# Kernel optimization log

Measured on AMD Instinct MI355X. Metric: run time of the kernel, lower is better.

## Reference

```python
import jax, jax.numpy as jnp
import numpy as np
import math

D_MODEL = 1024
N_HEADS = 16
D_HEAD = 64
GROUP_SIZE = 2
N_GROUPS = N_HEADS // GROUP_SIZE
D_MLP = 4096
BATCH = 2
SEQ = 2048
LN_EPS = 1e-5


def setup_inputs() -> dict:
    key = jax.random.key(0)
    ks = jax.random.split(key, 12)

    def xavier(k, shape):
        # torch xavier_uniform on a 3D tensor treats dim0 as fan_in, prod(rest) as fan_out
        fan_in = shape[0]
        fan_out = int(np.prod(shape[1:]))
        bound = math.sqrt(6.0 / (fan_in + fan_out))
        return jax.random.uniform(k, shape, jnp.float32, -bound, bound)

    def linear_w(k, out_f, in_f):
        bound = 1.0 / math.sqrt(in_f)
        return jax.random.uniform(k, (out_f, in_f), jnp.float32, -bound, bound)

    return {
        "x": jax.random.normal(ks[0], (BATCH, SEQ, D_MODEL), jnp.float32),
        "ln1_w": jnp.ones((D_MODEL,), jnp.float32),
        "ln1_b": jnp.zeros((D_MODEL,), jnp.float32),
        "W_Q": xavier(ks[1], (D_MODEL, N_HEADS, D_HEAD)),
        "W_K": xavier(ks[2], (D_MODEL, N_GROUPS, D_HEAD)),
        "W_V": xavier(ks[3], (D_MODEL, N_GROUPS, D_HEAD)),
        "W_out": xavier(ks[4], (D_HEAD, N_HEADS, D_MODEL)),
        "b_out": jnp.zeros((D_MODEL,), jnp.float32),
        "ln2_w": jnp.ones((D_MODEL,), jnp.float32),
        "ln2_b": jnp.zeros((D_MODEL,), jnp.float32),
        "mlp1_w": linear_w(ks[5], D_MLP, D_MODEL),
        "mlp1_b": jax.random.uniform(ks[6], (D_MLP,), jnp.float32, -1.0 / math.sqrt(D_MODEL), 1.0 / math.sqrt(D_MODEL)),
        "mlp2_w": linear_w(ks[7], D_MODEL, D_MLP),
        "mlp2_b": jax.random.uniform(ks[8], (D_MODEL,), jnp.float32, -1.0 / math.sqrt(D_MLP), 1.0 / math.sqrt(D_MLP)),
    }


def _layernorm(x, w, b):
    mu = jnp.mean(x, axis=-1, keepdims=True)
    var = jnp.var(x, axis=-1, keepdims=True)
    return (x - mu) * jax.lax.rsqrt(var + LN_EPS) * w + b


def _gqa_attention(resid, W_Q, W_K, W_V, W_out, b_out):
    b, s, _ = resid.shape
    q = jnp.einsum("bsd,dhk->bshk", resid, W_Q)            # [b, s, n_heads, d_head]
    q = q.reshape(b, s, N_GROUPS, GROUP_SIZE, D_HEAD)      # [b, s, g, gs, k]
    k = jnp.einsum("bsd,dgk->bsgk", resid, W_K)            # [b, s, g, k]
    v = jnp.einsum("bsd,dgk->bsgk", resid, W_V)
    scores = jnp.einsum("bqgik,btgk->bgiqt", q, k) / math.sqrt(D_HEAD)  # [b, g, gs, q, t]
    causal_mask = jnp.triu(jnp.ones((s, s), dtype=bool), k=1)
    scores = jnp.where(causal_mask, jnp.float32(-1000000.0), scores)
    probs = jax.nn.softmax(scores, axis=-1)
    z = jnp.einsum("bgiqt,btgk->bqgik", probs, v)          # [b, q, g, gs, k]
    z = z.reshape(b, s, N_HEADS, D_HEAD)
    return jnp.einsum("bshk,khd->bsd", z, W_out) + b_out


def reference(x, ln1_w, ln1_b, W_Q, W_K, W_V, W_out, b_out,
              ln2_w, ln2_b, mlp1_w, mlp1_b, mlp2_w, mlp2_b):
    normed = _layernorm(x, ln1_w, ln1_b)
    attn_out = _gqa_attention(normed, W_Q, W_K, W_V, W_out, b_out)
    post_attn = x + attn_out
    h = _layernorm(post_attn, ln2_w, ln2_b)
    h = jax.nn.gelu(h @ mlp1_w.T + mlp1_b, approximate=False)  # torch nn.GELU default = exact erf
    mlp_out = h @ mlp2_w.T + mlp2_b
    return post_attn + mlp_out
```

## Files before the change

### kernel.cpp

```cpp
#include <hip/hip_runtime.h>
#include <cstdint>
#include <cstddef>

typedef __attribute__((ext_vector_type(8))) short short8;
typedef __attribute__((ext_vector_type(4))) float f32x4;
typedef unsigned short u16;

#define MFMA16(a, b, c) __builtin_amdgcn_mfma_f32_16x16x32_bf16((a), (b), (c), 0, 0, 0)
#define SCL2 0.18033688011112042f

__device__ __forceinline__ u16 f2bf(float f) {
  union { float f; unsigned u; } c; c.f = f;
  unsigned r = c.u + 0x7fffu + ((c.u >> 16) & 1u);
  return (u16)(r >> 16);
}

__device__ __forceinline__ unsigned cvtpk(float a, float b) {
  unsigned r;
  asm("v_cvt_pk_bf16_f32 %0, %1, %2" : "=v"(r) : "v"(a), "v"(b));
  return r;
}


__global__ __launch_bounds__(256) void prep_wqkv(const float* __restrict__ wq,
    const float* __restrict__ wk, const float* __restrict__ wv, u16* __restrict__ outp)
{
  __shared__ float t[32][33];
  const int tx = threadIdx.x & 31, ty = threadIdx.x >> 5;
  const int n0 = blockIdx.x * 32, d0 = blockIdx.y * 32;
  const float* src; int stride, nc;
  if (n0 < 1024)      { src = wq; stride = 1024; nc = n0; }
  else if (n0 < 1536) { src = wk; stride = 512;  nc = n0 - 1024; }
  else                { src = wv; stride = 512;  nc = n0 - 1536; }
#pragma unroll
  for (int i = 0; i < 32; i += 8)
    t[ty + i][tx] = src[(size_t)(d0 + ty + i) * stride + nc + tx];
  __syncthreads();
#pragma unroll
  for (int i = 0; i < 32; i += 8)
    outp[(size_t)(n0 + ty + i) * 1024 + d0 + tx] = f2bf(t[tx][ty + i]);
}

__global__ __launch_bounds__(256) void prep_wout(const float* __restrict__ wo, u16* __restrict__ outp)
{
  __shared__ float t[32][33];
  const int tx = threadIdx.x & 31, ty = threadIdx.x >> 5;
  const int d0 = blockIdx.x * 32, c0 = blockIdx.y * 32;
#pragma unroll
  for (int i = 0; i < 32; i += 8) {
    int c = c0 + ty + i;
    t[ty + i][tx] = wo[(size_t)(c & 63) * 16384 + (size_t)(c >> 6) * 1024 + d0 + tx];
  }
  __syncthreads();
#pragma unroll
  for (int i = 0; i < 32; i += 8)
    outp[(size_t)(d0 + ty + i) * 1024 + c0 + tx] = f2bf(t[tx][ty + i]);
}

__global__ void convert_bf16(const float4* __restrict__ in, u16* __restrict__ out, int n4) {
  int i = blockIdx.x * 256 + threadIdx.x;
  if (i >= n4) return;
  float4 v = in[i];
  ushort4 o; o.x = f2bf(v.x); o.y = f2bf(v.y); o.z = f2bf(v.z); o.w = f2bf(v.w);
  ((ushort4*)out)[i] = o;
}

__global__ __launch_bounds__(256) void vt_transpose(const u16* __restrict__ qkv, u16* __restrict__ vtp)
{
  __shared__ u16 t[32][33];
  const int tx = threadIdx.x & 31, ty = threadIdx.x >> 5;
  const int t0 = blockIdx.x * 32, k0 = blockIdx.y * 32;
  const int bg = blockIdx.z, b = bg >> 3, g = bg & 7;
#pragma unroll
  for (int i = 0; i < 32; i += 8)
    t[ty + i][tx] = qkv[(size_t)(b * 2048 + t0 + ty + i) * 2048 + 1536 + g * 64 + k0 + tx];
  __syncthreads();
#pragma unroll
  for (int i = 0; i < 32; i += 8)
    vtp[(size_t)(bg * 64 + k0 + ty + i) * 2048 + t0 + tx] = t[tx][ty + i];
}

__global__ __launch_bounds__(256) void ln_bf16(const float* __restrict__ x,
    const float* __restrict__ w, const float* __restrict__ b, u16* __restrict__ out)
{
  const int row = blockIdx.x, tid = threadIdx.x;
  const float4 v = ((const float4*)(x + (size_t)row * 1024))[tid];
  float s = v.x + v.y + v.z + v.w;
  float s2 = v.x * v.x + v.y * v.y + v.z * v.z + v.w * v.w;
#pragma unroll
  for (int m = 32; m >= 1; m >>= 1) { s += __shfl_xor(s, m); s2 += __shfl_xor(s2, m); }
  __shared__ float red[8];
  if ((tid & 63) == 0) { red[tid >> 6] = s; red[4 + (tid >> 6)] = s2; }
  __syncthreads();
  s  = red[0] + red[1] + red[2] + red[3];
  s2 = red[4] + red[5] + red[6] + red[7];
  const float mu = s * (1.f / 1024.f);
  const float inv = rsqrtf(s2 * (1.f / 1024.f) - mu * mu + 1e-5f);
  const float4 wv = ((const float4*)w)[tid];
  const float4 bv = ((const float4*)b)[tid];
  ushort4 o;
  o.x = f2bf((v.x - mu) * inv * wv.x + bv.x);
  o.y = f2bf((v.y - mu) * inv * wv.y + bv.y);
  o.z = f2bf((v.z - mu) * inv * wv.z + bv.z);
  o.w = f2bf((v.w - mu) * inv * wv.w + bv.w);
  ((ushort4*)out)[(size_t)row * 256 + tid] = o;
}

#define BM 128
#define BN 128
#define BK 32

template<int EPI>
__global__ __launch_bounds__(256, 2) void gemm_bt(
    const u16* __restrict__ A, const u16* __restrict__ Bt, void* __restrict__ Cout,
    const float* __restrict__ bias, const float* __restrict__ resid,
    int M, int N, int K)
{
  __shared__ u16 As[4][BM * BK];
  __shared__ u16 Bs[4][BN * BK];
  const int tid = threadIdx.x;
  const int w = tid >> 6, lane = tid & 63;
  const int lo = lane & 15, hi = lane >> 4;
  const int mBase = blockIdx.x * BM, nBase = blockIdx.y * BN;
  const int wr = (w >> 1) * 64, wc = (w & 1) * 64;

  const f32x4 vzero = {0.f, 0.f, 0.f, 0.f};
  f32x4 acc[4][4];
#pragma unroll
  for (int i = 0; i < 4; ++i)
#pragma unroll
    for (int j = 0; j < 4; ++j) acc[i][j] = vzero;

  const int base0 = w * 2048 + lane * 16;
  int srow[2], skb[2];
#pragma unroll
  for (int c = 0; c < 2; ++c) {
    const int off = base0 + c * 1024;
    srow[c] = off >> 6;
    skb[c] = (off & 63) >> 1;
  }

  const int NT = K >> 5;

  auto stage = [&](int kt) {
    const int slot = kt & 3;
    const int k0 = kt * BK;
#pragma unroll
    for (int c = 0; c < 2; ++c) {
      const u16* ga = A  + (size_t)(mBase + srow[c]) * K + k0 + skb[c];
      const u16* gb = Bt + (size_t)(nBase + srow[c]) * K + k0 + skb[c];
      __builtin_amdgcn_global_load_lds((const __attribute__((address_space(1))) void*)ga,
          (__attribute__((address_space(3))) void*)((char*)&As[slot][0] + w * 2048 + c * 1024), 16, 0, 0);
      __builtin_amdgcn_global_load_lds((const __attribute__((address_space(1))) void*)gb,
          (__attribute__((address_space(3))) void*)((char*)&Bs[slot][0] + w * 2048 + c * 1024), 16, 0, 0);
    }
  };

  stage(0);
  stage(1);

  for (int kt = 0; kt < NT; ++kt) {
    if (kt + 2 < NT) {
      stage(kt + 2);
      asm volatile("s_waitcnt vmcnt(8)" ::: "memory");
    } else if (kt + 1 < NT) {
      asm volatile("s_waitcnt vmcnt(4)" ::: "memory");
    } else {
      asm volatile("s_waitcnt vmcnt(0)" ::: "memory");
    }
    __builtin_amdgcn_s_barrier();
    __builtin_amdgcn_sched_barrier(0);

    const int slot = kt & 3;
    short8 af[4], bf[4];
#pragma unroll
    for (int i = 0; i < 4; ++i) {
      af[i] = *(const short8*)((const char*)&As[slot][0] + (wr + i * 16 + lo) * 64 + hi * 16);
      bf[i] = *(const short8*)((const char*)&Bs[slot][0] + (wc + i * 16 + lo) * 64 + hi * 16);
    }
    __builtin_amdgcn_s_setprio(1);
#pragma unroll
    for (int i = 0; i < 4; ++i)
#pragma unroll
      for (int j = 0; j < 4; ++j)
        acc[i][j] = MFMA16(af[i], bf[j], acc[i][j]);
    __builtin_amdgcn_s_setprio(0);
  }

#pragma unroll
  for (int i = 0; i < 4; ++i) {
#pragma unroll
    for (int j = 0; j < 4; ++j) {
#pragma unroll
      for (int r = 0; r < 4; ++r) {
        const int row = mBase + wr + i * 16 + hi * 4 + r;
        const int col = nBase + wc + j * 16 + lo;
        float v = acc[i][j][r];
        if (EPI == 1 || EPI == 2) v += bias[col];
        if (EPI == 1) v += resid[(size_t)row * N + col];
        if (EPI == 2) v = 0.5f * v * (1.f + erff(v * 0.70710678118f));
        if (EPI == 3 && col < 1024) v *= SCL2;
        if (EPI == 1) ((float*)Cout)[(size_t)row * N + col] = v;
        else          ((u16*)Cout)[(size_t)row * N + col] = f2bf(v);
      }
    }
  }
}

template<int EPI>
__global__ __launch_bounds__(512, 2) void gemm256(
    const u16* __restrict__ A, const u16* __restrict__ Bt, void* __restrict__ Cout,
    const float* __restrict__ bias, const float* __restrict__ resid,
    int M, int N, int K)
{
  __shared__ u16 lds8[2][2][2][8192];
  const int tid = threadIdx.x;
  const int lane = tid & 63, lo = lane & 15, hi = lane >> 4;
  const int wid = tid >> 6, wr = wid >> 2, wc = wid & 3;
  const int mBase = blockIdx.x * 256, nBase = blockIdx.y * 256;
  const int sw = (lo & 7) << 4;

  const f32x4 vzero = {0.f, 0.f, 0.f, 0.f};
  f32x4 acc[8][4];
#pragma unroll
  for (int i = 0; i < 8; ++i)
#pragma unroll
    for (int j = 0; j < 4; ++j) acc[i][j] = vzero;

  int srow[2], scol[2];
#pragma unroll
  for (int c = 0; c < 2; ++c) {
    const int p = c * 8192 + tid * 16;
    const int r = p >> 7, bb = p & 127;
    srow[c] = r;
    scol[c] = (bb ^ ((r & 7) << 4)) >> 1;
  }

  const int NT = K >> 6;

#pragma unroll
  for (int mat = 0; mat < 2; ++mat)
#pragma unroll
    for (int half = 0; half < 2; ++half)
#pragma unroll
      for (int c = 0; c < 2; ++c) {
        const u16* g = (mat == 0)
          ? A  + (size_t)(mBase + half * 128 + srow[c]) * K + scol[c]
          : Bt + (size_t)(nBase + half * 128 + srow[c]) * K + scol[c];
        __builtin_amdgcn_global_load_lds((const __attribute__((address_space(1))) void*)g,
            (__attribute__((address_space(3))) void*)(&lds8[0][mat][half][c * 4096 + tid * 8]), 16, 0, 0);
      }
  asm volatile("s_waitcnt vmcnt(0)" ::: "memory");
  asm volatile("s_barrier" ::: "memory");

  for (int kt = 0; kt < NT; ++kt) {
    const int cur = kt & 1;
    const char* baseA = (const char*)&lds8[cur][0][wr][0];
    const char* baseB = (const char*)&lds8[cur][1][wc >> 1][0];
    const int rBB = (wc & 1) * 64;

    short8 bfr[4][2], afr[4][2];
#pragma unroll
    for (int nf = 0; nf < 4; ++nf)
#pragma unroll
      for (int ks = 0; ks < 2; ++ks)
        bfr[nf][ks] = *(const short8*)(baseB + (rBB + nf * 16 + lo) * 128 + ((ks * 64 + hi * 16) ^ sw));
#pragma unroll
    for (int mf = 0; mf < 4; ++mf)
#pragma unroll
      for (int ks = 0; ks < 2; ++ks)
        afr[mf][ks] = *(const short8*)(baseA + ((mf * 16 + lo) * 128 + ((ks * 64 + hi * 16) ^ sw)));

    if (kt + 1 < NT) {
      const int ko = (kt + 1) * 64;
#pragma unroll
      for (int mat = 0; mat < 2; ++mat)
#pragma unroll
        for (int half = 0; half < 2; ++half)
#pragma unroll
          for (int c = 0; c < 2; ++c) {
            const u16* g = (mat == 0)
              ? A  + (size_t)(mBase + half * 128 + srow[c]) * K + ko + scol[c]
              : Bt + (size_t)(nBase + half * 128 + srow[c]) * K + ko + scol[c];
            __builtin_amdgcn_global_load_lds((const __attribute__((address_space(1))) void*)g,
                (__attribute__((address_space(3))) void*)(&lds8[cur ^ 1][mat][half][c * 4096 + tid * 8]), 16, 0, 0);
          }
    }

    __builtin_amdgcn_s_setprio(1);
#pragma unroll
    for (int mf = 0; mf < 4; ++mf)
#pragma unroll
      for (int nf = 0; nf < 4; ++nf)
#pragma unroll
        for (int ks = 0; ks < 2; ++ks)
          acc[mf][nf] = MFMA16(afr[mf][ks], bfr[nf][ks], acc[mf][nf]);
    __builtin_amdgcn_s_setprio(0);

#pragma unroll
    for (int mf = 0; mf < 4; ++mf)
#pragma unroll
      for (int ks = 0; ks < 2; ++ks)
        afr[mf][ks] = *(const short8*)(baseA + (((mf + 4) * 16 + lo) * 128 + ((ks * 64 + hi * 16) ^ sw)));

    __builtin_amdgcn_s_setprio(1);
#pragma unroll
    for (int mf = 0; mf < 4; ++mf)
#pragma unroll
      for (int nf = 0; nf < 4; ++nf)
#pragma unroll
        for (int ks = 0; ks < 2; ++ks)
          acc[mf + 4][nf] = MFMA16(afr[mf][ks], bfr[nf][ks], acc[mf + 4][nf]);
    __builtin_amdgcn_s_setprio(0);

    asm volatile("s_waitcnt vmcnt(0)" ::: "memory");
    asm volatile("s_barrier" ::: "memory");
  }

#pragma unroll
  for (int mf = 0; mf < 8; ++mf) {
#pragma unroll
    for (int nf = 0; nf < 4; ++nf) {
#pragma unroll
      for (int r = 0; r < 4; ++r) {
        const int row = mBase + wr * 128 + mf * 16 + hi * 4 + r;
        const int col = nBase + wc * 64 + nf * 16 + lo;
        float v = acc[mf][nf][r];
        if (EPI != 0) v += bias[col];
        if (EPI == 1) v += resid[(size_t)row * N + col];
        if (EPI == 2) v = 0.5f * v * (1.f + erff(v * 0.70710678118f));
        if (EPI == 1) ((float*)Cout)[(size_t)row * N + col] = v;
        else          ((u16*)Cout)[(size_t)row * N + col] = f2bf(v);
      }
    }
  }
}

__global__ __launch_bounds__(256) void attn_fwd(const u16* __restrict__ qkv,
    const u16* __restrict__ vt, u16* __restrict__ z)
{
  __shared__ u16 Ks[2][64 * 64];
  __shared__ u16 Vs[2][64 * 64];
  __shared__ u16 Pl[4][32 * 72];
  const int tid = threadIdx.x;
  const int w = tid >> 6, lane = tid & 63, lo = lane & 15, hi = lane >> 4;
  const int bxr = blockIdx.x;
  const int chunk = (bxr & 1) ? (31 - (bxr >> 1)) : (bxr >> 1);
  const int bg = blockIdx.y, b = bg >> 3, g = bg & 7;
  const int h = (g << 1) | (w & 1);
  const int q0w = chunk * 64 + (w >> 1) * 32;
  const int sw = (lo & 7) << 4;

  short8 qA[2][2];
#pragma unroll
  for (int qf = 0; qf < 2; ++qf)
#pragma unroll
    for (int half = 0; half < 2; ++half)
      qA[qf][half] = *(const short8*)(qkv +
          (size_t)(b * 2048 + q0w + qf * 16 + lo) * 2048 + h * 64 + half * 32 + hi * 8);

  const f32x4 vzero = {0.f, 0.f, 0.f, 0.f};
  f32x4 zacc[2][4];
#pragma unroll
  for (int qf = 0; qf < 2; ++qf)
#pragma unroll
    for (int kf = 0; kf < 4; ++kf) zacc[qf][kf] = vzero;
  float lrun[2] = {0.f, 0.f};

  const u16* kbase = qkv + (size_t)b * 2048 * 2048 + 1024 + g * 64;
  const u16* vbase = vt + (size_t)(b * 8 + g) * 64 * 2048;

  int srow[2], scol[2];
#pragma unroll
  for (int c = 0; c < 2; ++c) {
    const int p = tid * 16 + c * 4096;
    const int r = p >> 7, bb = p & 127;
    srow[c] = r;
    scol[c] = (bb ^ ((r & 7) << 4)) >> 1;
  }

  const int nTiles = chunk + 1;
  u16* pw = &Pl[w][0];

  auto stageKV = [&](int it) {
    const int slot = it & 1;
    const int t0 = it * 64;
#pragma unroll
    for (int c = 0; c < 2; ++c) {
      __builtin_amdgcn_global_load_lds(
          (const __attribute__((address_space(1))) void*)(kbase + (size_t)(t0 + srow[c]) * 2048 + scol[c]),
          (__attribute__((address_space(3))) void*)((char*)&Ks[slot][0] + tid * 16 + c * 4096), 16, 0, 0);
      __builtin_amdgcn_global_load_lds(
          (const __attribute__((address_space(1))) void*)(vbase + (size_t)srow[c] * 2048 + t0 + scol[c]),
          (__attribute__((address_space(3))) void*)((char*)&Vs[slot][0] + tid * 16 + c * 4096), 16, 0, 0);
    }
  };

  stageKV(0);

  for (int it = 0; it < nTiles; ++it) {
    asm volatile("s_waitcnt vmcnt(0)" ::: "memory");
    __builtin_amdgcn_s_barrier();
    __builtin_amdgcn_sched_barrier(0);
    if (it + 1 < nTiles) stageKV(it + 1);

    const int slot = it & 1;
    const int ts = it * 64;
    const char* KsB = (const char*)&Ks[slot][0];
    const char* VsB = (const char*)&Vs[slot][0];

    short8 kA[4][2];
#pragma unroll
    for (int nt = 0; nt < 4; ++nt)
#pragma unroll
      for (int half = 0; half < 2; ++half)
        kA[nt][half] = *(const short8*)(KsB + (nt * 16 + lo) * 128 + ((half * 64 + hi * 16) ^ sw));

#pragma unroll
    for (int qf = 0; qf < 2; ++qf) {
      f32x4 p[4];
#pragma unroll
      for (int nt = 0; nt < 4; ++nt) {
        f32x4 t = MFMA16(kA[nt][0], qA[qf][0], vzero);
        p[nt] = MFMA16(kA[nt][1], qA[qf][1], t);
      }
      const int qrow0 = q0w + qf * 16;
      if (ts + 63 > qrow0) {
        const int rel = qrow0 + lo - ts;
#pragma unroll
        for (int nt = 0; nt < 4; ++nt)
#pragma unroll
          for (int r = 0; r < 4; ++r)
            if (nt * 16 + hi * 4 + r > rel) p[nt][r] = -1e30f;
      }
#pragma unroll
      for (int nt = 0; nt < 4; ++nt)
#pragma unroll
        for (int r = 0; r < 4; ++r) p[nt][r] = exp2f(p[nt][r]);
      float s0 = (p[0][0] + p[0][1]) + (p[0][2] + p[0][3]);
      float s1 = (p[1][0] + p[1][1]) + (p[1][2] + p[1][3]);
      float s2 = (p[2][0] + p[2][1]) + (p[2][2] + p[2][3]);
      float s3 = (p[3][0] + p[3][1]) + (p[3][2] + p[3][3]);
      lrun[qf] += (s0 + s1) + (s2 + s3);
#pragma unroll
      for (int nt = 0; nt < 4; ++nt) {
        uint2 uu;
        uu.x = cvtpk(p[nt][0], p[nt][1]);
        uu.y = cvtpk(p[nt][2], p[nt][3]);
        *(uint2*)((char*)pw + (qf * 16 + lo) * 144 + nt * 32 + hi * 8) = uu;
      }
    }
    asm volatile("s_waitcnt lgkmcnt(0)" ::: "memory");
    short8 pa[2][2];
#pragma unroll
    for (int qf = 0; qf < 2; ++qf)
#pragma unroll
      for (int tc = 0; tc < 2; ++tc)
        pa[qf][tc] = *(const short8*)((const char*)pw + (qf * 16 + lo) * 144 + tc * 64 + hi * 16);
#pragma unroll
    for (int kf = 0; kf < 4; ++kf) {
#pragma unroll
      for (int tc = 0; tc < 2; ++tc) {
        const short8 vf = *(const short8*)(VsB + (kf * 16 + lo) * 128 + ((tc * 64 + hi * 16) ^ sw));
        zacc[0][kf] = MFMA16(vf, pa[0][tc], zacc[0][kf]);
        zacc[1][kf] = MFMA16(vf, pa[1][tc], zacc[1][kf]);
      }
    }
  }

  u16* zp = z + (size_t)(b * 2048 + q0w) * 1024 + h * 64;
#pragma unroll
  for (int qf = 0; qf < 2; ++qf) {
    float rs = lrun[qf];
    rs += __shfl_xor(rs, 16);
    rs += __shfl_xor(rs, 32);
    const float inv = 1.f / rs;
#pragma unroll
    for (int kf = 0; kf < 4; ++kf) {
      uint2 o;
      o.x = cvtpk(zacc[qf][kf][0] * inv, zacc[qf][kf][1] * inv);
      o.y = cvtpk(zacc[qf][kf][2] * inv, zacc[qf][kf][3] * inv);
      *(uint2*)(zp + (size_t)(qf * 16 + lo) * 1024 + kf * 16 + hi * 4) = o;
    }
  }
}


extern "C" void kernel_launch(void* const* d_in, const int* in_sizes, int n_in,
                              void* d_out, int out_size, void* d_ws, size_t ws_size,
                              hipStream_t stream)
{
  (void)in_sizes; (void)n_in; (void)out_size; (void)ws_size;
  const float* x      = (const float*)d_in[0];
  const float* ln1_w  = (const float*)d_in[1];
  const float* ln1_b  = (const float*)d_in[2];
  const float* W_Q    = (const float*)d_in[3];
  const float* W_K    = (const float*)d_in[4];
  const float* W_V    = (const float*)d_in[5];
  const float* W_out  = (const float*)d_in[6];
  const float* b_out  = (const float*)d_in[7];
  const float* ln2_w  = (const float*)d_in[8];
  const float* ln2_b  = (const float*)d_in[9];
  const float* mlp1_w = (const float*)d_in[10];
  const float* mlp1_b = (const float*)d_in[11];
  const float* mlp2_w = (const float*)d_in[12];
  const float* mlp2_b = (const float*)d_in[13];
  float* out = (float*)d_out;

  char* ws = (char*)d_ws;
  u16*   wqkv_t = (u16*)(ws + 0);
  u16*   wout_t = (u16*)(ws + 4194304);
  u16*   w1     = (u16*)(ws + 6291456);
  u16*   w2     = (u16*)(ws + 14680064);
  u16*   normed = (u16*)(ws + 23068672);
  float* post   = (float*)(ws + 31457280);
  u16*   qkv    = (u16*)(ws + 48234496);
  u16*   vtb    = (u16*)(ws + 65011712);
  u16*   zb     = (u16*)(ws + 69206016);
  u16*   hbuf   = (u16*)(ws + 48234496);

  prep_wqkv<<<dim3(64, 32), 256, 0, stream>>>(W_Q, W_K, W_V, wqkv_t);
  prep_wout<<<dim3(32, 32), 256, 0, stream>>>(W_out, wout_t);
  convert_bf16<<<4096, 256, 0, stream>>>((const float4*)mlp1_w, w1, 1048576);
  convert_bf16<<<4096, 256, 0, stream>>>((const float4*)mlp2_w, w2, 1048576);

  ln_bf16<<<4096, 256, 0, stream>>>(x, ln1_w, ln1_b, normed);
  gemm_bt<3><<<dim3(32, 16), 256, 0, stream>>>(normed, wqkv_t, qkv, nullptr, nullptr, 4096, 2048, 1024);
  vt_transpose<<<dim3(64, 2, 16), 256, 0, stream>>>(qkv, vtb);
  attn_fwd<<<dim3(32, 16), 256, 0, stream>>>(qkv, vtb, zb);
  gemm_bt<1><<<dim3(32, 8), 256, 0, stream>>>(zb, wout_t, post, b_out, x, 4096, 1024, 1024);
  ln_bf16<<<4096, 256, 0, stream>>>(post, ln2_w, ln2_b, normed);
  gemm256<2><<<dim3(16, 16), 512, 0, stream>>>(normed, w1, hbuf, mlp1_b, nullptr, 4096, 4096, 1024);
  gemm_bt<1><<<dim3(32, 8), 256, 0, stream>>>(hbuf, w2, out, mlp2_b, post, 4096, 1024, 4096);
}
```

Baseline: 269.5 us.

## Split long causal attention chunks across two blocks and combine partials

```diff
diff --git a/kernel.cpp b/kernel.cpp
--- a/kernel.cpp
+++ b/kernel.cpp
@@ -13,6 +13,11 @@
   union { float f; unsigned u; } c; c.f = f;
   unsigned r = c.u + 0x7fffu + ((c.u >> 16) & 1u);
   return (u16)(r >> 16);
+}
+
+__device__ __forceinline__ float bf2f(u16 x) {
+  union { unsigned u; float f; } c; c.u = ((unsigned)x) << 16;
+  return c.f;
 }
 
 __device__ __forceinline__ unsigned cvtpk(float a, float b) {
@@ -337,15 +342,19 @@
 }
 
 __global__ __launch_bounds__(256) void attn_fwd(const u16* __restrict__ qkv,
-    const u16* __restrict__ vt, u16* __restrict__ z)
+    const u16* __restrict__ vt, u16* __restrict__ z,
+    u16* __restrict__ zscr, float* __restrict__ lscr)
 {
   __shared__ u16 Ks[2][64 * 64];
   __shared__ u16 Vs[2][64 * 64];
   __shared__ u16 Pl[4][32 * 72];
   const int tid = threadIdx.x;
   const int w = tid >> 6, lane = tid & 63, lo = lane & 15, hi = lane >> 4;
-  const int bxr = blockIdx.x;
-  const int chunk = (bxr & 1) ? (31 - (bxr >> 1)) : (bxr >> 1);
+  const int bx = blockIdx.x;
+  int chunk, itBeg, itEnd, mode;
+  if (bx < 16)      { chunk = bx;      itBeg = 0;  itEnd = chunk + 1; mode = 0; }
+  else if (bx < 32) { chunk = bx;      itBeg = 0;  itEnd = 16;        mode = 1; }
+  else              { chunk = bx - 16; itBeg = 16; itEnd = chunk + 1; mode = 2; }
   const int bg = blockIdx.y, b = bg >> 3, g = bg & 7;
   const int h = (g << 1) | (w & 1);
   const int q0w = chunk * 64 + (w >> 1) * 32;
@@ -379,7 +388,6 @@
     scol[c] = (bb ^ ((r & 7) << 4)) >> 1;
   }
 
-  const int nTiles = chunk + 1;
   u16* pw = &Pl[w][0];
 
   auto stageKV = [&](int it) {
@@ -396,13 +404,13 @@
     }
   };
 
-  stageKV(0);
-
-  for (int it = 0; it < nTiles; ++it) {
+  stageKV(itBeg);
+
+  for (int it = itBeg; it < itEnd; ++it) {
     asm volatile("s_waitcnt vmcnt(0)" ::: "memory");
     __builtin_amdgcn_s_barrier();
     __builtin_amdgcn_sched_barrier(0);
-    if (it + 1 < nTiles) stageKV(it + 1);
+    if (it + 1 < itEnd) stageKV(it + 1);
 
     const int slot = it & 1;
     const int ts = it * 64;
@@ -468,20 +476,71 @@
     }
   }
 
-  u16* zp = z + (size_t)(b * 2048 + q0w) * 1024 + h * 64;
-#pragma unroll
-  for (int qf = 0; qf < 2; ++qf) {
-    float rs = lrun[qf];
-    rs += __shfl_xor(rs, 16);
-    rs += __shfl_xor(rs, 32);
-    const float inv = 1.f / rs;
-#pragma unroll
-    for (int kf = 0; kf < 4; ++kf) {
-      uint2 o;
-      o.x = cvtpk(zacc[qf][kf][0] * inv, zacc[qf][kf][1] * inv);
-      o.y = cvtpk(zacc[qf][kf][2] * inv, zacc[qf][kf][3] * inv);
-      *(uint2*)(zp + (size_t)(qf * 16 + lo) * 1024 + kf * 16 + hi * 4) = o;
-    }
+  if (mode == 0) {
+    u16* zp = z + (size_t)(b * 2048 + q0w) * 1024 + h * 64;
+#pragma unroll
+    for (int qf = 0; qf < 2; ++qf) {
+      float rs = lrun[qf];
+      rs += __shfl_xor(rs, 16);
+      rs += __shfl_xor(rs, 32);
+      const float inv = 1.f / rs;
+#pragma unroll
+      for (int kf = 0; kf < 4; ++kf) {
+        uint2 o;
+        o.x = cvtpk(zacc[qf][kf][0] * inv, zacc[qf][kf][1] * inv);
+        o.y = cvtpk(zacc[qf][kf][2] * inv, zacc[qf][kf][3] * inv);
+        *(uint2*)(zp + (size_t)(qf * 16 + lo) * 1024 + kf * 16 + hi * 4) = o;
+      }
+    }
+  } else {
+    const int seg = mode - 1;
+    const int ci = chunk - 16;
+    const int idx2 = (bg * 16 + ci) * 2 + (w & 1);
+    u16* zs = zscr + ((size_t)seg * 512 * 4096) + ((size_t)idx2 * 64 + (w >> 1) * 32) * 64;
+    float* ls = lscr + (size_t)seg * 512 * 64 + (size_t)idx2 * 64 + (w >> 1) * 32;
+#pragma unroll
+    for (int qf = 0; qf < 2; ++qf) {
+      float rs = lrun[qf];
+      rs += __shfl_xor(rs, 16);
+      rs += __shfl_xor(rs, 32);
+      if (hi == 0) ls[qf * 16 + lo] = rs;
+#pragma unroll
+      for (int kf = 0; kf < 4; ++kf) {
+        uint2 o;
+        o.x = cvtpk(zacc[qf][kf][0], zacc[qf][kf][1]);
+        o.y = cvtpk(zacc[qf][kf][2], zacc[qf][kf][3]);
+        *(uint2*)(zs + (size_t)(qf * 16 + lo) * 64 + kf * 16 + hi * 4) = o;
+      }
+    }
+  }
+}
+
+__global__ __launch_bounds__(256) void attn_combine(const u16* __restrict__ zscr,
+    const float* __restrict__ lscr, u16* __restrict__ z)
+{
+  const int bgci = blockIdx.x;
+  const int bg = bgci >> 4, ci = bgci & 15;
+  const int b = bg >> 3, g = bg & 7, chunk = 16 + ci;
+  const int tid = threadIdx.x;
+#pragma unroll
+  for (int j = 0; j < 4; ++j) {
+    const int v = tid + j * 256;
+    const int k8 = v & 7, row = (v >> 3) & 63, hh = v >> 9;
+    const size_t base = ((size_t)(bgci * 2 + hh) * 64 + row) * 64 + k8 * 8;
+    const short8 z0 = *(const short8*)(zscr + base);
+    const short8 z1 = *(const short8*)(zscr + (size_t)512 * 4096 + base);
+    const size_t lidx = (size_t)(bgci * 2 + hh) * 64 + row;
+    const float inv = 1.f / (lscr[lidx] + lscr[(size_t)512 * 64 + lidx]);
+    float a[8];
+#pragma unroll
+    for (int e = 0; e < 8; ++e)
+      a[e] = (bf2f((u16)z0[e]) + bf2f((u16)z1[e])) * inv;
+    uint4 o;
+    o.x = cvtpk(a[0], a[1]);
+    o.y = cvtpk(a[2], a[3]);
+    o.z = cvtpk(a[4], a[5]);
+    o.w = cvtpk(a[6], a[7]);
+    *(uint4*)(z + ((size_t)(b * 2048 + chunk * 64 + row)) * 1024 + (g * 2 + hh) * 64 + k8 * 8) = o;
   }
 }
 
@@ -518,6 +577,8 @@
   u16*   vtb    = (u16*)(ws + 65011712);
   u16*   zb     = (u16*)(ws + 69206016);
   u16*   hbuf   = (u16*)(ws + 48234496);
+  u16*   zscr   = (u16*)(ws + 31457280);
+  float* lscr   = (float*)(ws + 23068672);
 
   prep_wqkv<<<dim3(64, 32), 256, 0, stream>>>(W_Q, W_K, W_V, wqkv_t);
   prep_wout<<<dim3(32, 32), 256, 0, stream>>>(W_out, wout_t);
@@ -527,7 +588,8 @@
   ln_bf16<<<4096, 256, 0, stream>>>(x, ln1_w, ln1_b, normed);
   gemm_bt<3><<<dim3(32, 16), 256, 0, stream>>>(normed, wqkv_t, qkv, nullptr, nullptr, 4096, 2048, 1024);
   vt_transpose<<<dim3(64, 2, 16), 256, 0, stream>>>(qkv, vtb);
-  attn_fwd<<<dim3(32, 16), 256, 0, stream>>>(qkv, vtb, zb);
+  attn_fwd<<<dim3(48, 16), 256, 0, stream>>>(qkv, vtb, zb, zscr, lscr);
+  attn_combine<<<256, 256, 0, stream>>>(zscr, lscr, zb);
   gemm_bt<1><<<dim3(32, 8), 256, 0, stream>>>(zb, wout_t, post, b_out, x, 4096, 1024, 1024);
   ln_bf16<<<4096, 256, 0, stream>>>(post, ln2_w, ln2_b, normed);
   gemm256<2><<<dim3(16, 16), 512, 0, stream>>>(normed, w1, hbuf, mlp1_b, nullptr, 4096, 4096, 1024);
```

New measurement: 261.6 us. -2.9%, faster.
